# Optimization experiments

Measured on AMD Instinct MI355X. Metric: run time of the kernel, lower is better.

## Reference

```python
import jax, jax.numpy as jnp
import numpy as np

B, T, S, N, C, H = 2, 16, 256, 32, 3072, 24
D = C // H  # 128 head_dim
EPS = 1e-6


def _layernorm(x):
    # LayerNorm, elementwise_affine=False, eps=1e-6
    mu = jnp.mean(x, axis=-1, keepdims=True)
    var = jnp.mean(jnp.square(x - mu), axis=-1, keepdims=True)
    return (x - mu) * jax.lax.rsqrt(var + EPS)


def _rmsnorm(x, w):
    # RMSNorm with learnable weight, computed in fp32 (matches x.float() path)
    ms = jnp.mean(jnp.square(x), axis=-1, keepdims=True)
    return x * jax.lax.rsqrt(ms + EPS) * w


def setup_inputs() -> dict:
    key = jax.random.key(0)
    ks = jax.random.split(key, 8)
    f = lambda k, sh: jax.random.normal(k, sh, dtype=jnp.float32)
    sc = 1.0 / np.sqrt(C)
    return {
        "x": f(ks[0], (B, T * S, C)),
        "motion_vec": f(ks[1], (B, T, N, C)),
        "motion_mask": jax.random.uniform(ks[2], (B, T * S), dtype=jnp.float32),
        "w_kv": f(ks[3], (2 * C, C)) * sc,
        "b_kv": jnp.zeros((2 * C,), jnp.float32),
        "w_q": f(ks[4], (C, C)) * sc,
        "b_q": jnp.zeros((C,), jnp.float32),
        "w_o": f(ks[5], (C, C)) * sc,
        "b_o": jnp.zeros((C,), jnp.float32),
        "q_norm_w": jnp.ones((D,), jnp.float32),
        "k_norm_w": jnp.ones((D,), jnp.float32),
    }


def reference(x, motion_vec, motion_mask, w_kv, b_kv, w_q, b_q, w_o, b_o,
              q_norm_w, k_norm_w):
    x_motion = _layernorm(motion_vec)            # [B,T,N,C]
    x_feat = _layernorm(x)                       # [B,T*S,C]

    kv = x_motion @ w_kv.T + b_kv                # [B,T,N,2C]
    kv = kv.reshape(B, T, N, 2, H, D)
    k, v = kv[:, :, :, 0], kv[:, :, :, 1]        # [B,T,N,H,D]

    q = (x_feat @ w_q.T + b_q).reshape(B, T, S, H, D)
    q = _rmsnorm(q, q_norm_w)
    k = _rmsnorm(k, k_norm_w)

    # frame-local cross-attention: queries = spatial tokens, keys = motion tokens
    scale = 1.0 / jnp.sqrt(jnp.float32(D))
    scores = jnp.einsum('btshd,btnhd->bthsn', q, k) * scale  # [B,T,H,S,N]
    probs = jax.nn.softmax(scores, axis=-1)
    attn = jnp.einsum('bthsn,btnhd->btshd', probs, v)        # [B,T,S,H,D]
    attn = attn.reshape(B, T * S, C)

    out = attn @ w_o.T + b_o                     # [B,T*S,C]
    return out * motion_mask[:, :, None]
```

## Files before the change

### kernel.cpp

```cpp
#include <hip/hip_runtime.h>
#include <math.h>

typedef unsigned short u16;
typedef unsigned int u32;
typedef short bf16x8 __attribute__((ext_vector_type(8)));
typedef float f32x4 __attribute__((ext_vector_type(4)));
typedef u16 u16x4 __attribute__((ext_vector_type(4)));
typedef u16 u16x8 __attribute__((ext_vector_type(8)));
typedef u32 u32x4 __attribute__((ext_vector_type(4)));

static __device__ __forceinline__ float b2f(u16 u) {
  union { u32 i; float f; } v; v.i = ((u32)u) << 16; return v.f;
}
static __device__ __forceinline__ u16 f2b(float f) {
  union { float f; u32 i; } v; v.f = f;
  u32 r = v.i + 0x7fffu + ((v.i >> 16) & 1u);
  return (u16)(r >> 16);
}

static __device__ __forceinline__ void g2l16(const void* g, void* l) {
  typedef __attribute__((address_space(1))) const void gvoid;
  typedef __attribute__((address_space(3))) void lvoid;
  __builtin_amdgcn_global_load_lds((gvoid*)g, (lvoid*)l, 16, 0, 0);
}

__global__ __launch_bounds__(256)
void wcvt_kernel(const float* __restrict__ src, u16* __restrict__ dst, int n4)
{
  for (int i = blockIdx.x * 256 + threadIdx.x; i < n4; i += gridDim.x * 256) {
    f32x4 v = *(const f32x4*)(src + (size_t)i * 4);
    u16x4 w; w.x = f2b(v.x); w.y = f2b(v.y); w.z = f2b(v.z); w.w = f2b(v.w);
    *(u16x4*)(dst + (size_t)i * 4) = w;
  }
}

__global__ __launch_bounds__(256)
void ln_kernel(const float* __restrict__ x, const float* __restrict__ mv,
               u16* __restrict__ xf, u16* __restrict__ xm)
{
  const int row = blockIdx.x, tid = threadIdx.x;
  const float* src; u16* dst;
  if (row < 8192) { src = x + (size_t)row * 3072;          dst = xf + (size_t)row * 3072; }
  else            { src = mv + (size_t)(row - 8192) * 3072; dst = xm + (size_t)(row - 8192) * 3072; }

  f32x4 vals[3];
  #pragma unroll
  for (int i = 0; i < 3; ++i) vals[i] = *(const f32x4*)(src + tid * 4 + i * 1024);

  float s1 = 0.f, s2 = 0.f;
  #pragma unroll
  for (int i = 0; i < 3; ++i) {
    f32x4 v = vals[i];
    s1 += v.x + v.y + v.z + v.w;
    s2 += v.x * v.x + v.y * v.y + v.z * v.z + v.w * v.w;
  }
  #pragma unroll
  for (int o = 32; o > 0; o >>= 1) { s1 += __shfl_down(s1, o); s2 += __shfl_down(s2, o); }
  __shared__ float r1[4], r2[4];
  const int wv = tid >> 6, ln = tid & 63;
  if (ln == 0) { r1[wv] = s1; r2[wv] = s2; }
  __syncthreads();
  const float t1 = r1[0] + r1[1] + r1[2] + r1[3];
  const float t2 = r2[0] + r2[1] + r2[2] + r2[3];
  const float mu = t1 * (1.f / 3072.f);
  const float rs = rsqrtf(t2 * (1.f / 3072.f) - mu * mu + 1e-6f);
  #pragma unroll
  for (int i = 0; i < 3; ++i) {
    f32x4 v = vals[i]; u16x4 w;
    w.x = f2b((v.x - mu) * rs); w.y = f2b((v.y - mu) * rs);
    w.z = f2b((v.z - mu) * rs); w.w = f2b((v.w - mu) * rs);
    *(u16x4*)(dst + tid * 4 + i * 1024) = w;
  }
}

template<int EPI, typename TOUT>
__global__ __launch_bounds__(256, 2)
void gemm256(const u16* __restrict__ A, const u16* __restrict__ Wb,
             const float* __restrict__ bias, const float* __restrict__ mask,
             TOUT* __restrict__ C, int M, int N, int K)
{
  __shared__ __align__(16) u16 L[36864];
  const int tid = threadIdx.x, wave = tid >> 6, lane = tid & 63;

  const int nwg = gridDim.x;
  const int bid = (blockIdx.x & 7) * (nwg >> 3) + (blockIdx.x >> 3);
  const int nbx = N >> 7;
  const int brow = (bid / nbx) << 8;
  const int bcol = (bid % nbx) << 7;
  const int wr = wave >> 1, wc = wave & 1;

  const u16* gA = A + (size_t)brow * K;
  const u16* gB = Wb + (size_t)bcol * K;

  const int srow = tid >> 2;
  const int scol = 8 * ((lane & 3) ^ ((lane >> 3) & 3));
  const int rcoff = 8 * ((lane >> 4) ^ ((lane >> 1) & 3));

  f32x4 acc[8][4] = {};

  auto STAGE = [&](int b, int tk) {
    u16* bufA = &L[b * 12288];
    u16* bufB = bufA + 8192;
    const u16* srcA = gA + tk + scol;
    const u16* srcB = gB + tk + scol;
    #pragma unroll
    for (int j = 0; j < 4; ++j)
      g2l16(srcA + (size_t)(j * 64 + srow) * K, bufA + (j * 64 + wave * 16) * 32);
    #pragma unroll
    for (int j = 0; j < 2; ++j)
      g2l16(srcB + (size_t)(j * 64 + srow) * K, bufB + (j * 64 + wave * 16) * 32);
  };

  auto COMPUTE = [&](int b) {
    const u16* bufA = &L[b * 12288];
    const u16* bufB = bufA + 8192;
    bf16x8 af[8], bfv[4];
    #pragma unroll
    for (int m = 0; m < 8; ++m)
      af[m] = *(const bf16x8*)&bufA[(wr * 128 + m * 16 + (lane & 15)) * 32 + rcoff];
    #pragma unroll
    for (int n = 0; n < 4; ++n)
      bfv[n] = *(const bf16x8*)&bufB[(wc * 64 + n * 16 + (lane & 15)) * 32 + rcoff];
    __builtin_amdgcn_s_setprio(1);
    #pragma unroll
    for (int m = 0; m < 8; ++m)
      #pragma unroll
      for (int n = 0; n < 4; ++n)
        acc[m][n] = __builtin_amdgcn_mfma_f32_16x16x32_bf16(af[m], bfv[n], acc[m][n], 0, 0, 0);
    __builtin_amdgcn_s_setprio(0);
  };

  STAGE(0, 0);
  STAGE(1, 32);
  asm volatile("s_waitcnt vmcnt(6)" ::: "memory");
  __builtin_amdgcn_s_barrier();
  __builtin_amdgcn_sched_barrier(0);

  const int NT = K >> 5;
  int cur = 0;
  for (int t = 0; t < NT; ++t) {
    const bool pf = (t + 2) < NT;
    if (pf) {
      int nb = cur + 2; if (nb >= 3) nb -= 3;
      STAGE(nb, (t + 2) << 5);
    }
    COMPUTE(cur);
    if (pf) asm volatile("s_waitcnt vmcnt(6)" ::: "memory");
    else    asm volatile("s_waitcnt vmcnt(0)" ::: "memory");
    __builtin_amdgcn_s_barrier();
    __builtin_amdgcn_sched_barrier(0);
    if (++cur == 3) cur = 0;
  }

  #pragma unroll
  for (int m = 0; m < 8; ++m) {
    const int row = brow + wr * 128 + m * 16 + ((lane >> 4) << 2);
    #pragma unroll
    for (int n = 0; n < 4; ++n) {
      const int col = bcol + wc * 64 + n * 16 + (lane & 15);
      const float bv = bias[col];
      #pragma unroll
      for (int i = 0; i < 4; ++i) {
        float v = acc[m][n][i] + bv;
        if (EPI == 1) v *= mask[row + i];
        if constexpr (__is_same(TOUT, u16))
          C[(size_t)(row + i) * N + col] = f2b(v);
        else
          C[(size_t)(row + i) * N + col] = v;
      }
    }
  }
}

template<int EPI, typename TOUT>
__global__ __launch_bounds__(256)
void gemm_mixed(const u16* __restrict__ A, const float* __restrict__ W,
                const float* __restrict__ bias, const float* __restrict__ mask,
                TOUT* __restrict__ C, int M, int N, int K)
{
  __shared__ __align__(16) u16 lA[4096];
  __shared__ __align__(16) u16 lB[4096];
  const int tid = threadIdx.x, wave = tid >> 6, lane = tid & 63;
  const int nbx = N >> 7;
  const int brow = (blockIdx.x / nbx) << 7;
  const int bcol = (blockIdx.x % nbx) << 7;
  const int wr = wave >> 1, wc = wave & 1;

  f32x4 acc[4][4] = {};
  const u16* gA = A + (size_t)brow * K;
  const float* gB = W + (size_t)bcol * K;
  const int br = tid >> 1, bk0 = (tid & 1) << 4;
  const float* bsrc0 = gB + (size_t)br * K + bk0;
  u16* bdst = &lB[br * 32 + bk0];

  for (int tk = 0; tk < K; tk += 32) {
    #pragma unroll
    for (int j = 0; j < 2; ++j) {
      const int c = j * 256 + wave * 64 + lane;
      const int r = c >> 2, k8 = (c & 3) << 3;
      g2l16(gA + (size_t)r * K + tk + k8, (char*)lA + (size_t)(j * 256 + wave * 64) * 16);
    }
    {
      const float* src = bsrc0 + tk;
      #pragma unroll
      for (int j = 0; j < 4; ++j) {
        f32x4 v = *(const f32x4*)(src + 4 * j);
        u16x4 w; w.x = f2b(v.x); w.y = f2b(v.y); w.z = f2b(v.z); w.w = f2b(v.w);
        *(u16x4*)(bdst + 4 * j) = w;
      }
    }
    __syncthreads();

    bf16x8 af[4], bfr[4];
    #pragma unroll
    for (int m = 0; m < 4; ++m)
      af[m] = *(const bf16x8*)&lA[(wr * 64 + m * 16 + (lane & 15)) * 32 + ((lane >> 4) << 3)];
    #pragma unroll
    for (int n = 0; n < 4; ++n)
      bfr[n] = *(const bf16x8*)&lB[(wc * 64 + n * 16 + (lane & 15)) * 32 + ((lane >> 4) << 3)];
    #pragma unroll
    for (int m = 0; m < 4; ++m)
      #pragma unroll
      for (int n = 0; n < 4; ++n)
        acc[m][n] = __builtin_amdgcn_mfma_f32_16x16x32_bf16(af[m], bfr[n], acc[m][n], 0, 0, 0);
    __syncthreads();
  }

  #pragma unroll
  for (int m = 0; m < 4; ++m) {
    const int row = brow + wr * 64 + m * 16 + ((lane >> 4) << 2);
    #pragma unroll
    for (int n = 0; n < 4; ++n) {
      const int col = bcol + wc * 64 + n * 16 + (lane & 15);
      const float bv = bias[col];
      #pragma unroll
      for (int i = 0; i < 4; ++i) {
        float v = acc[m][n][i] + bv;
        if (EPI == 1) v *= mask[row + i];
        if constexpr (__is_same(TOUT, u16))
          C[(size_t)(row + i) * N + col] = f2b(v);
        else
          C[(size_t)(row + i) * N + col] = v;
      }
    }
  }
}

__global__ __launch_bounds__(256)
void attn_mfma(const u16* __restrict__ qb, const u16* __restrict__ kvb,
               const float* __restrict__ qw, const float* __restrict__ kw,
               u16* __restrict__ attnb)
{
  __shared__ __align__(16) u16 Kn[32 * 136];
  __shared__ __align__(16) u16 Vt[128 * 40];
  __shared__ __align__(16) u16 Pl[256 * 40];
  __shared__ __align__(16) u16 Ol[4][16 * 136];
  const int tid = threadIdx.x, wave = tid >> 6, lane = tid & 63;
  const int h = blockIdx.x % 24;
  const int bt = blockIdx.x / 24;

  {
    const int n = tid >> 3, sub = tid & 7;
    const size_t base = (size_t)(bt * 32 + n) * 6144 + (size_t)h * 128;
    const u16* kp = kvb + base + sub * 16;
    u16x8 k0 = *(const u16x8*)kp;
    u16x8 k1 = *(const u16x8*)(kp + 8);
    float kv_[16]; float ss = 0.f;
    #pragma unroll
    for (int j = 0; j < 8; ++j) { kv_[j] = b2f(k0[j]); kv_[8 + j] = b2f(k1[j]); }
    #pragma unroll
    for (int j = 0; j < 16; ++j) ss += kv_[j] * kv_[j];
    ss += __shfl_xor(ss, 1); ss += __shfl_xor(ss, 2); ss += __shfl_xor(ss, 4);
    const float krs = rsqrtf(ss * (1.f / 128.f) + 1e-6f);
    u16x8 w0, w1;
    #pragma unroll
    for (int j = 0; j < 8; ++j) {
      const int d = sub * 16 + j;
      w0[j] = f2b(kv_[j] * krs * kw[d] * qw[d]);
      w1[j] = f2b(kv_[8 + j] * krs * kw[d + 8] * qw[d + 8]);
    }
    *(u16x8*)&Kn[n * 136 + sub * 16] = w0;
    *(u16x8*)&Kn[n * 136 + sub * 16 + 8] = w1;
  }
  {
    const int k = tid >> 3, dc = (tid & 7) * 16;
    const u16* vp = kvb + (size_t)(bt * 32 + k) * 6144 + (size_t)h * 128 + 3072 + dc;
    u16x8 v0 = *(const u16x8*)vp;
    u16x8 v1 = *(const u16x8*)(vp + 8);
    #pragma unroll
    for (int j = 0; j < 8; ++j) {
      Vt[(dc + j) * 40 + k] = v0[j];
      Vt[(dc + 8 + j) * 40 + k] = v1[j];
    }
  }
  __syncthreads();

  const int q0 = wave * 64;
  const int lr = lane & 15, lg = lane >> 4;

  for (int m = 0; m < 4; ++m) {
    const int qrow = q0 + m * 16 + lr;
    const u16* qp = qb + (size_t)(bt * 256 + qrow) * 3072 + (size_t)h * 128 + lg * 8;
    bf16x8 qf[4];
    #pragma unroll
    for (int k = 0; k < 4; ++k) qf[k] = *(const bf16x8*)(qp + k * 32);
    float ss = 0.f;
    #pragma unroll
    for (int k = 0; k < 4; ++k)
      #pragma unroll
      for (int j = 0; j < 8; ++j) { const float f = b2f((u16)qf[k][j]); ss += f * f; }
    ss += __shfl_xor(ss, 16); ss += __shfl_xor(ss, 32);
    const float qsc = rsqrtf(ss * (1.f / 128.f) + 1e-6f) * 0.08838834764831845f;
    #pragma unroll
    for (int k = 0; k < 4; ++k)
      #pragma unroll
      for (int j = 0; j < 8; ++j)
        qf[k][j] = (short)f2b(b2f((u16)qf[k][j]) * qsc);

    f32x4 s0 = {0.f, 0.f, 0.f, 0.f}, s1 = {0.f, 0.f, 0.f, 0.f};
    #pragma unroll
    for (int k = 0; k < 4; ++k) {
      bf16x8 kb0 = *(const bf16x8*)&Kn[(lr) * 136 + k * 32 + lg * 8];
      bf16x8 kb1 = *(const bf16x8*)&Kn[(16 + lr) * 136 + k * 32 + lg * 8];
      s0 = __builtin_amdgcn_mfma_f32_16x16x32_bf16(qf[k], kb0, s0, 0, 0, 0);
      s1 = __builtin_amdgcn_mfma_f32_16x16x32_bf16(qf[k], kb1, s1, 0, 0, 0);
    }

    float mx[4], sm[4], e0[4], e1[4];
    #pragma unroll
    for (int i = 0; i < 4; ++i) mx[i] = fmaxf(s0[i], s1[i]);
    #pragma unroll
    for (int o = 1; o <= 8; o <<= 1)
      #pragma unroll
      for (int i = 0; i < 4; ++i) mx[i] = fmaxf(mx[i], __shfl_xor(mx[i], o));
    #pragma unroll
    for (int i = 0; i < 4; ++i) {
      e0[i] = __expf(s0[i] - mx[i]);
      e1[i] = __expf(s1[i] - mx[i]);
      sm[i] = e0[i] + e1[i];
    }
    #pragma unroll
    for (int o = 1; o <= 8; o <<= 1)
      #pragma unroll
      for (int i = 0; i < 4; ++i) sm[i] += __shfl_xor(sm[i], o);
    #pragma unroll
    for (int i = 0; i < 4; ++i) {
      const float inv = 1.f / sm[i];
      const int pr = (q0 + m * 16 + lg * 4 + i) * 40;
      Pl[pr + lr] = f2b(e0[i] * inv);
      Pl[pr + 16 + lr] = f2b(e1[i] * inv);
    }
    asm volatile("s_waitcnt lgkmcnt(0)" ::: "memory");
    __builtin_amdgcn_sched_barrier(0);

    bf16x8 pf = *(const bf16x8*)&Pl[(q0 + m * 16 + lr) * 40 + lg * 8];
    f32x4 o_[8];
    #pragma unroll
    for (int n = 0; n < 8; ++n) {
      bf16x8 vb = *(const bf16x8*)&Vt[(n * 16 + lr) * 40 + lg * 8];
      o_[n] = __builtin_amdgcn_mfma_f32_16x16x32_bf16(
                pf, vb, (f32x4){0.f, 0.f, 0.f, 0.f}, 0, 0, 0);
    }

    u16* ow = &Ol[wave][0];
    #pragma unroll
    for (int n = 0; n < 8; ++n)
      #pragma unroll
      for (int i = 0; i < 4; ++i)
        ow[(lg * 4 + i) * 136 + n * 16 + lr] = f2b(o_[n][i]);
    asm volatile("s_waitcnt lgkmcnt(0)" ::: "memory");
    __builtin_amdgcn_sched_barrier(0);
    const int r = lane >> 2, cc = (lane & 3) * 32;
    u16* gout = attnb + (size_t)(bt * 256 + q0 + m * 16 + r) * 3072 + (size_t)h * 128 + cc;
    #pragma unroll
    for (int c = 0; c < 4; ++c)
      *(u16x8*)(gout + c * 8) = *(const u16x8*)&ow[r * 136 + cc + c * 8];
    asm volatile("s_waitcnt lgkmcnt(0)" ::: "memory");
    __builtin_amdgcn_sched_barrier(0);
  }
}

extern "C" void kernel_launch(void* const* d_in, const int* in_sizes, int n_in,
                              void* d_out, int out_size, void* d_ws, size_t ws_size,
                              hipStream_t stream) {
  const float* x    = (const float*)d_in[0];
  const float* mv   = (const float*)d_in[1];
  const float* mask = (const float*)d_in[2];
  const float* wkv  = (const float*)d_in[3];
  const float* bkv  = (const float*)d_in[4];
  const float* wq   = (const float*)d_in[5];
  const float* bq   = (const float*)d_in[6];
  const float* wo   = (const float*)d_in[7];
  const float* bo   = (const float*)d_in[8];
  const float* qnw  = (const float*)d_in[9];
  const float* knw  = (const float*)d_in[10];
  float* out = (float*)d_out;

  char* ws = (char*)d_ws;
  u16* xf   = (u16*)(ws);
  u16* xm   = (u16*)(ws + 50331648);
  u16* qbuf = (u16*)(ws + 56623104);
  u16* kvb  = (u16*)(ws + 106954752);
  u16* wslab = (u16*)(ws + 119537664);

  ln_kernel<<<9216, 256, 0, stream>>>(x, mv, xf, xm);

  if (ws_size >= 157286400u) {
    wcvt_kernel<<<2048, 256, 0, stream>>>(wq, wslab, 3072 * 3072 / 4);
    gemm256<0, u16><<<768, 256, 0, stream>>>(xf, wslab, bq, nullptr, qbuf, 8192, 3072, 3072);
    wcvt_kernel<<<2048, 256, 0, stream>>>(wkv, wslab, 6144 * 3072 / 4);
    gemm256<0, u16><<<192, 256, 0, stream>>>(xm, wslab, bkv, nullptr, kvb, 1024, 6144, 3072);
    attn_mfma<<<768, 256, 0, stream>>>(qbuf, kvb, qnw, knw, xf);
    wcvt_kernel<<<2048, 256, 0, stream>>>(wo, wslab, 3072 * 3072 / 4);
    gemm256<1, float><<<768, 256, 0, stream>>>(xf, wslab, bo, mask, out, 8192, 3072, 3072);
  } else {
    gemm_mixed<0, u16><<<1536, 256, 0, stream>>>(xf, wq, bq, nullptr, qbuf, 8192, 3072, 3072);
    gemm_mixed<0, u16><<<384, 256, 0, stream>>>(xm, wkv, bkv, nullptr, kvb, 1024, 6144, 3072);
    attn_mfma<<<768, 256, 0, stream>>>(qbuf, kvb, qnw, knw, xf);
    gemm_mixed<1, float><<<1536, 256, 0, stream>>>(xf, wo, bo, mask, out, 8192, 3072, 3072);
  }
}
```

Before: 475.5 us.

## Use 256x256-tile 512-thread triple-buffered GEMM for Q and output projections

Adds a GEMM kernel with square 256x256 output tiles, 8 waves per block and a three-stage LDS ring with prefetch split across two MFMA half-steps. It replaces the 256x128 kernel for the Q and output projections. The aim is to raise arithmetic intensity per LDS/global load and hide load latency. In exchange the grid shrinks to 384 blocks with 96KB LDS each, which may cause wave-quantization tail and lower occupancy.

```diff
diff --git a/kernel.cpp b/kernel.cpp
--- a/kernel.cpp
+++ b/kernel.cpp
@@ -70,6 +70,123 @@
     w.x = f2b((v.x - mu) * rs); w.y = f2b((v.y - mu) * rs);
     w.z = f2b((v.z - mu) * rs); w.w = f2b((v.w - mu) * rs);
     *(u16x4*)(dst + tid * 4 + i * 1024) = w;
+  }
+}
+
+template<int EPI, typename TOUT>
+__global__ __launch_bounds__(512, 2)
+void gemm256sq(const u16* __restrict__ A, const u16* __restrict__ Wb,
+               const float* __restrict__ bias, const float* __restrict__ mask,
+               TOUT* __restrict__ C, int M, int N, int K)
+{
+  __shared__ __align__(16) u16 L[49152];
+  const int tid = threadIdx.x, wave = tid >> 6, lane = tid & 63;
+  const int wr = wave >> 2, wc = wave & 3;
+
+  const int nwg = gridDim.x;
+  const int bid = (blockIdx.x & 7) * (nwg >> 3) + (blockIdx.x >> 3);
+  const int nbx = N >> 8;
+  const int brow = (bid / nbx) << 8;
+  const int bcol = (bid % nbx) << 8;
+
+  const u16* gA = A + (size_t)brow * K;
+  const u16* gB = Wb + (size_t)bcol * K;
+
+  const int srow = tid >> 2;
+  const int scol = 8 * ((lane & 3) ^ ((lane >> 3) & 3));
+  const int rcoff = 8 * ((lane >> 4) ^ ((lane >> 1) & 3));
+  const int lr = lane & 15;
+
+  f32x4 acc[8][4] = {};
+
+  auto SGA = [&](int b, int tk) {
+    u16* buf = &L[b * 16384];
+    const u16* src = gA + tk + scol;
+    #pragma unroll
+    for (int j = 0; j < 2; ++j)
+      g2l16(src + (size_t)(j * 128 + srow) * K, buf + (j * 128 + wave * 16) * 32);
+  };
+  auto SGB = [&](int b, int tk) {
+    u16* buf = &L[b * 16384 + 8192];
+    const u16* src = gB + tk + scol;
+    #pragma unroll
+    for (int j = 0; j < 2; ++j)
+      g2l16(src + (size_t)(j * 128 + srow) * K, buf + (j * 128 + wave * 16) * 32);
+  };
+
+  SGA(0, 0); SGB(0, 0);
+  SGA(1, 32); SGB(1, 32);
+  asm volatile("s_waitcnt vmcnt(4)" ::: "memory");
+  __builtin_amdgcn_s_barrier();
+  __builtin_amdgcn_sched_barrier(0);
+
+  const int NT = K >> 5;
+  int cur = 0;
+  for (int t = 0; t < NT; ++t) {
+    const bool pf = (t + 2) < NT;
+    int nb = cur + 2; if (nb >= 3) nb -= 3;
+    const int ptk = (t + 2) << 5;
+    const u16* bufA = &L[cur * 16384];
+    const u16* bufB = bufA + 8192;
+
+    bf16x8 bfv[4], af[4];
+    #pragma unroll
+    for (int n = 0; n < 4; ++n)
+      bfv[n] = *(const bf16x8*)&bufB[(wc * 64 + n * 16 + lr) * 32 + rcoff];
+    #pragma unroll
+    for (int m = 0; m < 4; ++m)
+      af[m] = *(const bf16x8*)&bufA[(wr * 128 + m * 16 + lr) * 32 + rcoff];
+    if (pf) SGA(nb, ptk);
+    __builtin_amdgcn_s_barrier();
+    asm volatile("s_waitcnt lgkmcnt(0)" ::: "memory");
+    __builtin_amdgcn_sched_barrier(0);
+    __builtin_amdgcn_s_setprio(1);
+    #pragma unroll
+    for (int m = 0; m < 4; ++m)
+      #pragma unroll
+      for (int n = 0; n < 4; ++n)
+        acc[m][n] = __builtin_amdgcn_mfma_f32_16x16x32_bf16(af[m], bfv[n], acc[m][n], 0, 0, 0);
+    __builtin_amdgcn_s_setprio(0);
+    __builtin_amdgcn_s_barrier();
+
+    #pragma unroll
+    for (int m = 0; m < 4; ++m)
+      af[m] = *(const bf16x8*)&bufA[(wr * 128 + (m + 4) * 16 + lr) * 32 + rcoff];
+    if (pf) SGB(nb, ptk);
+    __builtin_amdgcn_s_barrier();
+    asm volatile("s_waitcnt lgkmcnt(0)" ::: "memory");
+    __builtin_amdgcn_sched_barrier(0);
+    __builtin_amdgcn_s_setprio(1);
+    #pragma unroll
+    for (int m = 0; m < 4; ++m)
+      #pragma unroll
+      for (int n = 0; n < 4; ++n)
+        acc[m + 4][n] = __builtin_amdgcn_mfma_f32_16x16x32_bf16(af[m], bfv[n], acc[m + 4][n], 0, 0, 0);
+    __builtin_amdgcn_s_setprio(0);
+    if (pf) asm volatile("s_waitcnt vmcnt(4)" ::: "memory");
+    else    asm volatile("s_waitcnt vmcnt(0)" ::: "memory");
+    __builtin_amdgcn_s_barrier();
+    __builtin_amdgcn_sched_barrier(0);
+    if (++cur == 3) cur = 0;
+  }
+
+  #pragma unroll
+  for (int m = 0; m < 8; ++m) {
+    const int row = brow + wr * 128 + m * 16 + ((lane >> 4) << 2);
+    #pragma unroll
+    for (int n = 0; n < 4; ++n) {
+      const int col = bcol + wc * 64 + n * 16 + lr;
+      const float bv = bias[col];
+      #pragma unroll
+      for (int i = 0; i < 4; ++i) {
+        float v = acc[m][n][i] + bv;
+        if (EPI == 1) v *= mask[row + i];
+        if constexpr (__is_same(TOUT, u16))
+          C[(size_t)(row + i) * N + col] = f2b(v);
+        else
+          C[(size_t)(row + i) * N + col] = v;
+      }
+    }
   }
 }
 
@@ -407,12 +524,12 @@
 
   if (ws_size >= 157286400u) {
     wcvt_kernel<<<2048, 256, 0, stream>>>(wq, wslab, 3072 * 3072 / 4);
-    gemm256<0, u16><<<768, 256, 0, stream>>>(xf, wslab, bq, nullptr, qbuf, 8192, 3072, 3072);
+    gemm256sq<0, u16><<<384, 512, 0, stream>>>(xf, wslab, bq, nullptr, qbuf, 8192, 3072, 3072);
     wcvt_kernel<<<2048, 256, 0, stream>>>(wkv, wslab, 6144 * 3072 / 4);
     gemm256<0, u16><<<192, 256, 0, stream>>>(xm, wslab, bkv, nullptr, kvb, 1024, 6144, 3072);
     attn_mfma<<<768, 256, 0, stream>>>(qbuf, kvb, qnw, knw, xf);
     wcvt_kernel<<<2048, 256, 0, stream>>>(wo, wslab, 3072 * 3072 / 4);
-    gemm256<1, float><<<768, 256, 0, stream>>>(xf, wslab, bo, mask, out, 8192, 3072, 3072);
+    gemm256sq<1, float><<<384, 512, 0, stream>>>(xf, wslab, bo, mask, out, 8192, 3072, 3072);
   } else {
     gemm_mixed<0, u16><<<1536, 256, 0, stream>>>(xf, wq, bq, nullptr, qbuf, 8192, 3072, 3072);
     gemm_mixed<0, u16><<<384, 256, 0, stream>>>(xm, wkv, bkv, nullptr, kvb, 1024, 6144, 3072);
```

Result: slower. 516.3 us (+8.6%).

## Fuse weight conversions into LN/attention kernels, merge Q/KV GEMMs, add 128x192 out-proj GEMM

Applied to the files above, without the earlier changes.

Folds the bf16 conversion of w_q and w_kv into the layernorm kernel as extra blocks, and the w_o conversion into the attention kernel as extra blocks. The Q and KV projections now run in one fused GEMM launch so the small KV GEMM shares the device with the Q GEMM. The output projection uses a new 128x192 tile GEMM with a triple-buffered async LDS pipeline and s_setprio around the MFMA loop. The goal is fewer launches, no idle tail from the small KV GEMM, and better tile balance across CUs. In exchange the default path needs a larger workspace and a different buffer layout, and w_o reuses the w_q slab after the Q GEMM has finished with it.

```diff
diff --git a/kernel.cpp b/kernel.cpp
--- a/kernel.cpp
+++ b/kernel.cpp
@@ -17,6 +17,11 @@
   u32 r = v.i + 0x7fffu + ((v.i >> 16) & 1u);
   return (u16)(r >> 16);
 }
+static __device__ __forceinline__ void cvt16(const float* src, u16* dst, int i) {
+  f32x4 v = *(const f32x4*)(src + (size_t)i * 4);
+  u16x4 w; w.x = f2b(v.x); w.y = f2b(v.y); w.z = f2b(v.z); w.w = f2b(v.w);
+  *(u16x4*)(dst + (size_t)i * 4) = w;
+}
 
 static __device__ __forceinline__ void g2l16(const void* g, void* l) {
   typedef __attribute__((address_space(1))) const void gvoid;
@@ -27,21 +32,30 @@
 __global__ __launch_bounds__(256)
 void wcvt_kernel(const float* __restrict__ src, u16* __restrict__ dst, int n4)
 {
-  for (int i = blockIdx.x * 256 + threadIdx.x; i < n4; i += gridDim.x * 256) {
-    f32x4 v = *(const f32x4*)(src + (size_t)i * 4);
-    u16x4 w; w.x = f2b(v.x); w.y = f2b(v.y); w.z = f2b(v.z); w.w = f2b(v.w);
-    *(u16x4*)(dst + (size_t)i * 4) = w;
-  }
+  for (int i = blockIdx.x * 256 + threadIdx.x; i < n4; i += gridDim.x * 256)
+    cvt16(src, dst, i);
 }
 
 __global__ __launch_bounds__(256)
-void ln_kernel(const float* __restrict__ x, const float* __restrict__ mv,
-               u16* __restrict__ xf, u16* __restrict__ xm)
-{
-  const int row = blockIdx.x, tid = threadIdx.x;
+void prep_kernel(const float* __restrict__ x, const float* __restrict__ mv,
+                 u16* __restrict__ xf, u16* __restrict__ xm,
+                 const float* __restrict__ wq, u16* __restrict__ wqs,
+                 const float* __restrict__ wkv, u16* __restrict__ wkvs)
+{
+  const int b = blockIdx.x, tid = threadIdx.x;
+  if (b >= 9216) {
+    if (b < 10240) {
+      const int n4 = 3072 * 3072 / 4;
+      for (int i = (b - 9216) * 256 + tid; i < n4; i += 1024 * 256) cvt16(wq, wqs, i);
+    } else {
+      const int n4 = 6144 * 3072 / 4;
+      for (int i = (b - 10240) * 256 + tid; i < n4; i += 1024 * 256) cvt16(wkv, wkvs, i);
+    }
+    return;
+  }
   const float* src; u16* dst;
-  if (row < 8192) { src = x + (size_t)row * 3072;          dst = xf + (size_t)row * 3072; }
-  else            { src = mv + (size_t)(row - 8192) * 3072; dst = xm + (size_t)(row - 8192) * 3072; }
+  if (b < 8192) { src = x + (size_t)b * 3072;          dst = xf + (size_t)b * 3072; }
+  else          { src = mv + (size_t)(b - 8192) * 3072; dst = xm + (size_t)(b - 8192) * 3072; }
 
   f32x4 vals[3];
   #pragma unroll
@@ -74,19 +88,15 @@
 }
 
 template<int EPI, typename TOUT>
-__global__ __launch_bounds__(256, 2)
-void gemm256(const u16* __restrict__ A, const u16* __restrict__ Wb,
-             const float* __restrict__ bias, const float* __restrict__ mask,
-             TOUT* __restrict__ C, int M, int N, int K)
-{
-  __shared__ __align__(16) u16 L[36864];
+static __device__ __forceinline__ void g256_body(
+    const u16* __restrict__ A, const u16* __restrict__ Wb,
+    const float* __restrict__ bias, const float* __restrict__ mask,
+    TOUT* __restrict__ C, int N, int K, int tb, u16* L)
+{
   const int tid = threadIdx.x, wave = tid >> 6, lane = tid & 63;
-
-  const int nwg = gridDim.x;
-  const int bid = (blockIdx.x & 7) * (nwg >> 3) + (blockIdx.x >> 3);
   const int nbx = N >> 7;
-  const int brow = (bid / nbx) << 8;
-  const int bcol = (bid % nbx) << 7;
+  const int brow = (tb / nbx) << 8;
+  const int bcol = (tb % nbx) << 7;
   const int wr = wave >> 1, wc = wave & 1;
 
   const u16* gA = A + (size_t)brow * K;
@@ -173,65 +183,120 @@
 }
 
 template<int EPI, typename TOUT>
-__global__ __launch_bounds__(256)
-void gemm_mixed(const u16* __restrict__ A, const float* __restrict__ W,
-                const float* __restrict__ bias, const float* __restrict__ mask,
-                TOUT* __restrict__ C, int M, int N, int K)
-{
-  __shared__ __align__(16) u16 lA[4096];
-  __shared__ __align__(16) u16 lB[4096];
+__global__ __launch_bounds__(256, 2)
+void gemm256(const u16* __restrict__ A, const u16* __restrict__ Wb,
+             const float* __restrict__ bias, const float* __restrict__ mask,
+             TOUT* __restrict__ C, int M, int N, int K)
+{
+  __shared__ __align__(16) u16 L[36864];
+  const int nwg = gridDim.x;
+  const int tb = (blockIdx.x & 7) * (nwg >> 3) + (blockIdx.x >> 3);
+  g256_body<EPI, TOUT>(A, Wb, bias, mask, C, N, K, tb, L);
+}
+
+__global__ __launch_bounds__(256, 2)
+void gemm_fused(const u16* __restrict__ Aq, const u16* __restrict__ Bq,
+                const float* __restrict__ bq, u16* __restrict__ Cq,
+                const u16* __restrict__ Akv, const u16* __restrict__ Bkv,
+                const float* __restrict__ bkv, u16* __restrict__ Ckv, int K)
+{
+  __shared__ __align__(16) u16 L[36864];
+  const int b0 = blockIdx.x;
+  if (b0 < 768) {
+    const int tb = (b0 & 7) * 96 + (b0 >> 3);
+    g256_body<0, u16>(Aq, Bq, bq, nullptr, Cq, 3072, K, tb, L);
+  } else {
+    const int b2 = b0 - 768;
+    const int tb = (b2 & 7) * 24 + (b2 >> 3);
+    g256_body<0, u16>(Akv, Bkv, bkv, nullptr, Ckv, 6144, K, tb, L);
+  }
+}
+
+template<int EPI, typename TOUT>
+__global__ __launch_bounds__(256, 2)
+void gemm192(const u16* __restrict__ A, const u16* __restrict__ Wb,
+             const float* __restrict__ bias, const float* __restrict__ mask,
+             TOUT* __restrict__ C, int M, int N, int K)
+{
+  __shared__ __align__(16) u16 L[30720];
   const int tid = threadIdx.x, wave = tid >> 6, lane = tid & 63;
-  const int nbx = N >> 7;
-  const int brow = (blockIdx.x / nbx) << 7;
-  const int bcol = (blockIdx.x % nbx) << 7;
+  const int nwg = gridDim.x;
+  const int tb = (blockIdx.x & 7) * (nwg >> 3) + (blockIdx.x >> 3);
+  const int nbx = N / 192;
+  const int brow = (tb / nbx) << 7;
+  const int bcol = (tb % nbx) * 192;
   const int wr = wave >> 1, wc = wave & 1;
 
-  f32x4 acc[4][4] = {};
   const u16* gA = A + (size_t)brow * K;
-  const float* gB = W + (size_t)bcol * K;
-  const int br = tid >> 1, bk0 = (tid & 1) << 4;
-  const float* bsrc0 = gB + (size_t)br * K + bk0;
-  u16* bdst = &lB[br * 32 + bk0];
-
-  for (int tk = 0; tk < K; tk += 32) {
-    #pragma unroll
-    for (int j = 0; j < 2; ++j) {
-      const int c = j * 256 + wave * 64 + lane;
-      const int r = c >> 2, k8 = (c & 3) << 3;
-      g2l16(gA + (size_t)r * K + tk + k8, (char*)lA + (size_t)(j * 256 + wave * 64) * 16);
-    }
-    {
-      const float* src = bsrc0 + tk;
-      #pragma unroll
-      for (int j = 0; j < 4; ++j) {
-        f32x4 v = *(const f32x4*)(src + 4 * j);
-        u16x4 w; w.x = f2b(v.x); w.y = f2b(v.y); w.z = f2b(v.z); w.w = f2b(v.w);
-        *(u16x4*)(bdst + 4 * j) = w;
-      }
-    }
-    __syncthreads();
-
-    bf16x8 af[4], bfr[4];
+  const u16* gB = Wb + (size_t)bcol * K;
+
+  const int srow = tid >> 2;
+  const int scol = 8 * ((lane & 3) ^ ((lane >> 3) & 3));
+  const int rcoff = 8 * ((lane >> 4) ^ ((lane >> 1) & 3));
+  const int lr = lane & 15;
+
+  f32x4 acc[4][6] = {};
+
+  auto STAGE = [&](int b, int tk) {
+    u16* bufA = &L[b * 10240];
+    u16* bufB = bufA + 4096;
+    const u16* srcA = gA + tk + scol;
+    const u16* srcB = gB + tk + scol;
+    #pragma unroll
+    for (int j = 0; j < 2; ++j)
+      g2l16(srcA + (size_t)(j * 64 + srow) * K, bufA + (j * 64 + wave * 16) * 32);
+    #pragma unroll
+    for (int j = 0; j < 3; ++j)
+      g2l16(srcB + (size_t)(j * 64 + srow) * K, bufB + (j * 64 + wave * 16) * 32);
+  };
+
+  auto COMPUTE = [&](int b) {
+    const u16* bufA = &L[b * 10240];
+    const u16* bufB = bufA + 4096;
+    bf16x8 af[4], bfv[6];
     #pragma unroll
     for (int m = 0; m < 4; ++m)
-      af[m] = *(const bf16x8*)&lA[(wr * 64 + m * 16 + (lane & 15)) * 32 + ((lane >> 4) << 3)];
-    #pragma unroll
-    for (int n = 0; n < 4; ++n)
-      bfr[n] = *(const bf16x8*)&lB[(wc * 64 + n * 16 + (lane & 15)) * 32 + ((lane >> 4) << 3)];
+      af[m] = *(const bf16x8*)&bufA[(wr * 64 + m * 16 + lr) * 32 + rcoff];
+    #pragma unroll
+    for (int n = 0; n < 6; ++n)
+      bfv[n] = *(const bf16x8*)&bufB[(wc * 96 + n * 16 + lr) * 32 + rcoff];
+    __builtin_amdgcn_s_setprio(1);
     #pragma unroll
     for (int m = 0; m < 4; ++m)
       #pragma unroll
-      for (int n = 0; n < 4; ++n)
-        acc[m][n] = __builtin_amdgcn_mfma_f32_16x16x32_bf16(af[m], bfr[n], acc[m][n], 0, 0, 0);
-    __syncthreads();
+      for (int n = 0; n < 6; ++n)
+        acc[m][n] = __builtin_amdgcn_mfma_f32_16x16x32_bf16(af[m], bfv[n], acc[m][n], 0, 0, 0);
+    __builtin_amdgcn_s_setprio(0);
+  };
+
+  STAGE(0, 0);
+  STAGE(1, 32);
+  asm volatile("s_waitcnt vmcnt(5)" ::: "memory");
+  __builtin_amdgcn_s_barrier();
+  __builtin_amdgcn_sched_barrier(0);
+
+  const int NT = K >> 5;
+  int cur = 0;
+  for (int t = 0; t < NT; ++t) {
+    const bool pf = (t + 2) < NT;
+    if (pf) {
+      int nb = cur + 2; if (nb >= 3) nb -= 3;
+      STAGE(nb, (t + 2) << 5);
+    }
+    COMPUTE(cur);
+    if (pf) asm volatile("s_waitcnt vmcnt(5)" ::: "memory");
+    else    asm volatile("s_waitcnt vmcnt(0)" ::: "memory");
+    __builtin_amdgcn_s_barrier();
+    __builtin_amdgcn_sched_barrier(0);
+    if (++cur == 3) cur = 0;
   }
 
   #pragma unroll
   for (int m = 0; m < 4; ++m) {
     const int row = brow + wr * 64 + m * 16 + ((lane >> 4) << 2);
     #pragma unroll
-    for (int n = 0; n < 4; ++n) {
-      const int col = bcol + wc * 64 + n * 16 + (lane & 15);
+    for (int n = 0; n < 6; ++n) {
+      const int col = bcol + wc * 96 + n * 16 + lr;
       const float bv = bias[col];
       #pragma unroll
       for (int i = 0; i < 4; ++i) {
@@ -246,16 +311,98 @@
   }
 }
 
+template<int EPI, typename TOUT>
 __global__ __launch_bounds__(256)
-void attn_mfma(const u16* __restrict__ qb, const u16* __restrict__ kvb,
+void gemm_mixed(const u16* __restrict__ A, const float* __restrict__ W,
+                const float* __restrict__ bias, const float* __restrict__ mask,
+                TOUT* __restrict__ C, int M, int N, int K)
+{
+  __shared__ __align__(16) u16 lA[4096];
+  __shared__ __align__(16) u16 lB[4096];
+  const int tid = threadIdx.x, wave = tid >> 6, lane = tid & 63;
+  const int nbx = N >> 7;
+  const int brow = (blockIdx.x / nbx) << 7;
+  const int bcol = (blockIdx.x % nbx) << 7;
+  const int wr = wave >> 1, wc = wave & 1;
+
+  f32x4 acc[4][4] = {};
+  const u16* gA = A + (size_t)brow * K;
+  const float* gB = W + (size_t)bcol * K;
+  const int br = tid >> 1, bk0 = (tid & 1) << 4;
+  const float* bsrc0 = gB + (size_t)br * K + bk0;
+  u16* bdst = &lB[br * 32 + bk0];
+
+  for (int tk = 0; tk < K; tk += 32) {
+    #pragma unroll
+    for (int j = 0; j < 2; ++j) {
+      const int c = j * 256 + wave * 64 + lane;
+      const int r = c >> 2, k8 = (c & 3) << 3;
+      g2l16(gA + (size_t)r * K + tk + k8, (char*)lA + (size_t)(j * 256 + wave * 64) * 16);
+    }
+    {
+      const float* src = bsrc0 + tk;
+      #pragma unroll
+      for (int j = 0; j < 4; ++j) {
+        f32x4 v = *(const f32x4*)(src + 4 * j);
+        u16x4 w; w.x = f2b(v.x); w.y = f2b(v.y); w.z = f2b(v.z); w.w = f2b(v.w);
+        *(u16x4*)(bdst + 4 * j) = w;
+      }
+    }
+    __syncthreads();
+
+    bf16x8 af[4], bfr[4];
+    #pragma unroll
+    for (int m = 0; m < 4; ++m)
+      af[m] = *(const bf16x8*)&lA[(wr * 64 + m * 16 + (lane & 15)) * 32 + ((lane >> 4) << 3)];
+    #pragma unroll
+    for (int n = 0; n < 4; ++n)
+      bfr[n] = *(const bf16x8*)&lB[(wc * 64 + n * 16 + (lane & 15)) * 32 + ((lane >> 4) << 3)];
+    #pragma unroll
+    for (int m = 0; m < 4; ++m)
+      #pragma unroll
+      for (int n = 0; n < 4; ++n)
+        acc[m][n] = __builtin_amdgcn_mfma_f32_16x16x32_bf16(af[m], bfr[n], acc[m][n], 0, 0, 0);
+    __syncthreads();
+  }
+
+  #pragma unroll
+  for (int m = 0; m < 4; ++m) {
+    const int row = brow + wr * 64 + m * 16 + ((lane >> 4) << 2);
+    #pragma unroll
+    for (int n = 0; n < 4; ++n) {
+      const int col = bcol + wc * 64 + n * 16 + (lane & 15);
+      const float bv = bias[col];
+      #pragma unroll
+      for (int i = 0; i < 4; ++i) {
+        float v = acc[m][n][i] + bv;
+        if (EPI == 1) v *= mask[row + i];
+        if constexpr (__is_same(TOUT, u16))
+          C[(size_t)(row + i) * N + col] = f2b(v);
+        else
+          C[(size_t)(row + i) * N + col] = v;
+      }
+    }
+  }
+}
+
+__global__ __launch_bounds__(256)
+void attn_wcvt(const u16* __restrict__ qb, const u16* __restrict__ kvb,
                const float* __restrict__ qw, const float* __restrict__ kw,
-               u16* __restrict__ attnb)
+               u16* __restrict__ attnb,
+               const float* __restrict__ wo, u16* __restrict__ wos)
 {
   __shared__ __align__(16) u16 Kn[32 * 136];
   __shared__ __align__(16) u16 Vt[128 * 40];
   __shared__ __align__(16) u16 Pl[256 * 40];
   __shared__ __align__(16) u16 Ol[4][16 * 136];
-  const int tid = threadIdx.x, wave = tid >> 6, lane = tid & 63;
+  const int tid = threadIdx.x;
+  if (blockIdx.x >= 768) {
+    const int n4 = 3072 * 3072 / 4;
+    for (int i = (blockIdx.x - 768) * 256 + tid; i < n4; i += 1024 * 256)
+      cvt16(wo, wos, i);
+    return;
+  }
+  const int wave = tid >> 6, lane = tid & 63;
   const int h = blockIdx.x % 24;
   const int bt = blockIdx.x / 24;
 
@@ -397,26 +544,45 @@
   float* out = (float*)d_out;
 
   char* ws = (char*)d_ws;
-  u16* xf   = (u16*)(ws);
-  u16* xm   = (u16*)(ws + 50331648);
-  u16* qbuf = (u16*)(ws + 56623104);
-  u16* kvb  = (u16*)(ws + 106954752);
-  u16* wslab = (u16*)(ws + 119537664);
-
-  ln_kernel<<<9216, 256, 0, stream>>>(x, mv, xf, xm);
-
-  if (ws_size >= 157286400u) {
+
+  if (ws_size >= 176160768u) {
+    u16* wqs  = (u16*)(ws);
+    u16* wkvs = (u16*)(ws + 18874368);
+    u16* xf   = (u16*)(ws + 56623104);
+    u16* xm   = (u16*)(ws + 106954752);
+    u16* qbuf = (u16*)(ws + 113246208);
+    u16* kvb  = (u16*)(ws + 163577856);
+    u16* wos  = wqs;
+
+    prep_kernel<<<11264, 256, 0, stream>>>(x, mv, xf, xm, wq, wqs, wkv, wkvs);
+    gemm_fused<<<960, 256, 0, stream>>>(xf, wqs, bq, qbuf, xm, wkvs, bkv, kvb, 3072);
+    attn_wcvt<<<1792, 256, 0, stream>>>(qbuf, kvb, qnw, knw, xf, wo, wos);
+    gemm192<1, float><<<1024, 256, 0, stream>>>(xf, wos, bo, mask, out, 8192, 3072, 3072);
+  } else if (ws_size >= 157286400u) {
+    u16* xf    = (u16*)(ws);
+    u16* xm    = (u16*)(ws + 50331648);
+    u16* qbuf  = (u16*)(ws + 56623104);
+    u16* kvb   = (u16*)(ws + 106954752);
+    u16* wslab = (u16*)(ws + 119537664);
+
+    prep_kernel<<<9216, 256, 0, stream>>>(x, mv, xf, xm, wq, wslab, wkv, wslab);
     wcvt_kernel<<<2048, 256, 0, stream>>>(wq, wslab, 3072 * 3072 / 4);
     gemm256<0, u16><<<768, 256, 0, stream>>>(xf, wslab, bq, nullptr, qbuf, 8192, 3072, 3072);
     wcvt_kernel<<<2048, 256, 0, stream>>>(wkv, wslab, 6144 * 3072 / 4);
     gemm256<0, u16><<<192, 256, 0, stream>>>(xm, wslab, bkv, nullptr, kvb, 1024, 6144, 3072);
-    attn_mfma<<<768, 256, 0, stream>>>(qbuf, kvb, qnw, knw, xf);
+    attn_wcvt<<<768, 256, 0, stream>>>(qbuf, kvb, qnw, knw, xf, wo, wslab);
     wcvt_kernel<<<2048, 256, 0, stream>>>(wo, wslab, 3072 * 3072 / 4);
-    gemm256<1, float><<<768, 256, 0, stream>>>(xf, wslab, bo, mask, out, 8192, 3072, 3072);
+    gemm192<1, float><<<1024, 256, 0, stream>>>(xf, wslab, bo, mask, out, 8192, 3072, 3072);
   } else {
+    u16* xf   = (u16*)(ws);
+    u16* xm   = (u16*)(ws + 50331648);
+    u16* qbuf = (u16*)(ws + 56623104);
+    u16* kvb  = (u16*)(ws + 106954752);
+
+    prep_kernel<<<9216, 256, 0, stream>>>(x, mv, xf, xm, wq, xf, wkv, xf);
     gemm_mixed<0, u16><<<1536, 256, 0, stream>>>(xf, wq, bq, nullptr, qbuf, 8192, 3072, 3072);
     gemm_mixed<0, u16><<<384, 256, 0, stream>>>(xm, wkv, bkv, nullptr, kvb, 1024, 6144, 3072);
-    attn_mfma<<<768, 256, 0, stream>>>(qbuf, kvb, qnw, knw, xf);
+    attn_wcvt<<<768, 256, 0, stream>>>(qbuf, kvb, qnw, knw, xf, wo, xf);
     gemm_mixed<1, float><<<1536, 256, 0, stream>>>(xf, wo, bo, mask, out, 8192, 3072, 3072);
   }
 }
```

Result: faster. 462.1 us (-2.8%).
